# Optimization experiments

Measured on AMD Instinct MI355X. Metric: run time of the kernel, lower is better.

The kernel has to match this reference:

```python
import jax, jax.numpy as jnp
import numpy as np

B, T, N, H, DH = 32, 64, 100, 4, 32  # batch, seq, nodes, heads, dim/head


def setup_inputs() -> dict:
    key = jax.random.key(0)
    ks = jax.random.split(key, 20)
    # structured flat observation: [action_mask(132), adj(100*100), dt(1), obs(256), siem(128)]
    am = (jax.random.uniform(ks[0], (B, T, 132)) < 0.8).astype(jnp.float32)
    adj = (jax.random.uniform(ks[1], (B, T, N * N)) < 0.05).astype(jnp.float32)
    dt = jax.random.uniform(ks[2], (B, T, 1)) * 0.1 + 0.01
    obs = jax.random.normal(ks[3], (B, T, 256))
    siem = jax.random.normal(ks[4], (B, T, 128))
    inputs = jnp.concatenate([am, adj, dt, obs, siem], axis=-1)
    s = 0.05
    return dict(
        inputs=inputs,
        h0=jnp.zeros((B, 128), jnp.float32),
        fc_w=jax.random.normal(ks[5], (384, 256)) * s,
        fc_b=jnp.zeros((256,)),
        gat_w=jax.random.normal(ks[6], (256, H, DH)) * s,
        a_src=jax.random.normal(ks[7], (H, DH)) * s,
        a_dst=jax.random.normal(ks[8], (H, DH)) * s,
        ode_w1=jax.random.normal(ks[9], (128, 128)) * s,
        ode_b1=jnp.zeros((128,)),
        ode_w2=jax.random.normal(ks[10], (128, 128)) * s,
        ode_b2=jnp.zeros((128,)),
        gru_wi=jax.random.normal(ks[11], (128, 384)) * s,
        gru_wh=jax.random.normal(ks[12], (128, 384)) * s,
        gru_bi=jnp.zeros((384,)),
        gru_bh=jnp.zeros((384,)),
        act_w=jax.random.normal(ks[13], (128, 132)) * s,
        act_b=jnp.zeros((132,)),
        val_w=jax.random.normal(ks[14], (128, 1)) * s,
        val_b=jnp.zeros((1,)),
    )


def reference(inputs, h0, fc_w, fc_b, gat_w, a_src, a_dst, ode_w1, ode_b1,
              ode_w2, ode_b2, gru_wi, gru_wh, gru_bi, gru_bh, act_w, act_b,
              val_w, val_b):
    Bt, Tt = inputs.shape[0], inputs.shape[1]
    action_mask = inputs[..., :132]
    adj_raw = inputs[..., 132:10132].reshape(Bt * Tt, N, N)
    dtn = inputs[..., 10132:10133]                      # [B,T,1]
    x = jnp.concatenate([inputs[..., 10133:10389], inputs[..., 10389:10517]], -1)
    x = jax.nn.relu(x @ fc_w + fc_b).reshape(Bt * Tt, 256)
    # SubnetMaskGenerator.create_mask: binary adjacency + self loops
    adj = (adj_raw > 0) | jnp.eye(N, dtype=bool)[None]
    # place per-agent embedding at node 0, rest zero
    x_nodes = jnp.zeros((Bt * Tt, N, 256), x.dtype).at[:, 0, :].set(x)
    Wh = jnp.einsum('bnf,fhd->bhnd', x_nodes, gat_w)
    src = jnp.einsum('bhnd,hd->bhn', Wh, a_src)
    dst = jnp.einsum('bhnd,hd->bhn', Wh, a_dst)
    e = jax.nn.leaky_relu(src[:, :, :, None] + dst[:, :, None, :], 0.2)
    e = jnp.where(adj[:, None, :, :], e, -1e9)
    alpha = jax.nn.softmax(e, axis=-1)
    hgat = jax.nn.elu(jnp.einsum('bhij,bhjd->bhid', alpha, Wh))
    hgat = hgat.transpose(0, 2, 1, 3).reshape(Bt * Tt, N, H * DH)
    x_gat = hgat.mean(axis=1).reshape(Bt, Tt, 128)

    def f(h):  # ODE dynamics net
        return jnp.tanh(jnp.tanh(h @ ode_w1 + ode_b1) @ ode_w2 + ode_b2)

    def step(h, inp):
        xt, dt = inp                                    # [B,128], [B,1]
        k1 = f(h)
        k2 = f(h + 0.5 * dt * k1)
        k3 = f(h + 0.5 * dt * k2)
        k4 = f(h + dt * k3)
        h_ode = h + dt / 6.0 * (k1 + 2 * k2 + 2 * k3 + k4)
        gi = xt @ gru_wi + gru_bi
        gh = h_ode @ gru_wh + gru_bh
        ir, iz, inn = jnp.split(gi, 3, -1)
        hr, hz, hn = jnp.split(gh, 3, -1)
        r = jax.nn.sigmoid(ir + hr)
        z = jax.nn.sigmoid(iz + hz)
        n = jnp.tanh(inn + r * hn)
        h_new = (1.0 - z) * n + z * h_ode
        return h_new, h_new

    h_T, hs = jax.lax.scan(step, h0, (x_gat.transpose(1, 0, 2), dtn.transpose(1, 0, 2)))
    x_rnn = hs.transpose(1, 0, 2)                       # [B,T,128]
    logits = x_rnn @ act_w + act_b
    value = (x_rnn @ val_w + val_b).reshape(-1)
    masked_logits = jnp.where(action_mask == 0.0, jnp.float32(-1e10), logits)
    return masked_logits, h_T, value
```

## Files before the change

### kernel.cpp

```cpp
#include <hip/hip_runtime.h>

#define NIN 10517
typedef unsigned short ushort_t;
using f32x4  = __attribute__((ext_vector_type(4))) float;
using bf16x8 = __attribute__((ext_vector_type(8))) short;

__device__ __forceinline__ float lrelu02(float x){ return x > 0.f ? x : 0.2f*x; }
__device__ __forceinline__ float fast_tanh(float x){ float e=__expf(2.f*x); return 1.f - 2.f/(e+1.f); }
__device__ __forceinline__ float fast_sig(float x){ return 1.f/(1.f+__expf(-x)); }

__device__ __forceinline__ ushort_t f2bf(float x){
  unsigned u = __float_as_uint(x);
  unsigned r = u + 0x7FFF + ((u >> 16) & 1);
  return (ushort_t)(r >> 16);
}

#define LBAR() do { asm volatile("s_waitcnt lgkmcnt(0)" ::: "memory"); \
                    __builtin_amdgcn_s_barrier(); } while (0)

__global__ __launch_bounds__(256) void k_fc_gat(const float* __restrict__ inputs,
    const float* __restrict__ fc_w, const float* __restrict__ fc_b,
    const float* __restrict__ gat_w, const float* __restrict__ a_src, const float* __restrict__ a_dst,
    const float* __restrict__ ode_w1, const float* __restrict__ ode_w2, const float* __restrict__ gru_wh,
    float* __restrict__ wh0_ws, float* __restrict__ sd_ws,
    ushort_t* __restrict__ w1B, ushort_t* __restrict__ w2B, ushort_t* __restrict__ ghB)
{
  __shared__ float xin[16][384];
  __shared__ float xfc[16][256];
  __shared__ float wh[16][128];
  const int tid = threadIdx.x;
  const int bt0 = blockIdx.x * 16;

  {
    int gidx = blockIdx.x * 256 + tid;
    for (int idx = gidx; idx < 384*128; idx += 128*256) {
      int m = idx >> 7, k = idx & 127;
      ghB[idx] = f2bf(gru_wh[k*384 + m]);
    }
    if (gidx < 128*128) {
      int jj = gidx >> 7, k = gidx & 127;
      w1B[gidx] = f2bf(ode_w1[k*128 + jj]);
      w2B[gidx] = f2bf(ode_w2[k*128 + jj]);
    }
  }

  for (int idx = tid; idx < 16*384; idx += 256) {
    int r = idx / 384, f = idx - r*384;
    xin[r][f] = inputs[(size_t)(bt0+r)*NIN + 10133 + f];
  }
  __syncthreads();
  {
    float acc[16];
    float bj = fc_b[tid];
    #pragma unroll
    for (int r=0;r<16;r++) acc[r] = bj;
    for (int f=0; f<384; f++) {
      float wf = fc_w[f*256 + tid];
      #pragma unroll
      for (int r=0;r<16;r++) acc[r] = fmaf(xin[r][f], wf, acc[r]);
    }
    #pragma unroll
    for (int r=0;r<16;r++) xfc[r][tid] = fmaxf(acc[r], 0.f);
  }
  __syncthreads();
  {
    const int j2 = tid & 127, r0 = (tid >> 7) * 8;
    float acc[8];
    #pragma unroll
    for (int r=0;r<8;r++) acc[r] = 0.f;
    for (int f=0; f<256; f++) {
      float wf = gat_w[f*128 + j2];
      #pragma unroll
      for (int r=0;r<8;r++) acc[r] = fmaf(xfc[r0+r][f], wf, acc[r]);
    }
    #pragma unroll
    for (int r=0;r<8;r++) {
      wh[r0+r][j2] = acc[r];
      wh0_ws[(size_t)(bt0+r0+r)*128 + j2] = acc[r];
    }
  }
  __syncthreads();
  if (tid < 128) {
    const int r = tid >> 3, h = (tid >> 1) & 3, w = tid & 1;
    const float* av = w ? a_dst : a_src;
    float acc = 0.f;
    #pragma unroll
    for (int d=0; d<32; d++) acc = fmaf(wh[r][h*32+d], av[h*32+d], acc);
    sd_ws[(size_t)(bt0+r)*8 + w*4 + h] = acc;
  }
}

__global__ __launch_bounds__(256) void k_alpha_gi(const float* __restrict__ inputs,
    const float* __restrict__ wh0_ws, const float* __restrict__ sd_ws,
    const float* __restrict__ gru_wi, const float* __restrict__ gru_bi,
    float* __restrict__ gi_ws)
{
  __shared__ int cnt[100];
  __shared__ int a0f[100];
  __shared__ float alpha[4][100];
  __shared__ float wh0[128];
  __shared__ float sdl[8];
  __shared__ float xg[128];
  const int tid = threadIdx.x;
  const size_t bt = blockIdx.x;
  if (tid < 128) wh0[tid] = wh0_ws[bt*128 + tid];
  if (tid < 8) sdl[tid] = sd_ws[bt*8 + tid];
  const float* adj = inputs + bt*NIN + 132;
  const int wv = tid >> 6, lane = tid & 63;
  for (int i = wv; i < 100; i += 4) {
    float v0 = adj[i*100 + lane];
    int pred0 = (lane != 0) && ((v0 > 0.f) || (lane == i));
    unsigned long long b0 = __ballot(pred0);
    int pred1 = 0;
    if (lane < 36) {
      float v1 = adj[i*100 + 64 + lane];
      pred1 = (v1 > 0.f) || ((64 + lane) == i);
    }
    unsigned long long b1 = __ballot(pred1);
    if (lane == 0) {
      cnt[i] = __popcll(b0) + __popcll(b1);
      a0f[i] = (v0 > 0.f) ? 1 : 0;
    }
  }
  __syncthreads();
  for (int idx = tid; idx < 400; idx += 256) {
    int h = idx / 100, i = idx - h*100;
    float s = sdl[h], d = sdl[4+h];
    float a;
    if (i == 0) {
      float ea = __expf(lrelu02(s + d));
      float eb = __expf(lrelu02(s));
      a = ea / (ea + (float)cnt[0] * eb);
    } else if (a0f[i]) {
      float ed = __expf(lrelu02(d));
      a = ed / (ed + (float)cnt[i]);
    } else {
      a = 0.f;
    }
    alpha[h][i] = a;
  }
  __syncthreads();
  if (tid < 128) {
    const int h = tid >> 5;
    const float w = wh0[tid];
    float sum = 0.f;
    for (int i=0;i<100;i++) {
      float t = alpha[h][i] * w;
      sum += (t > 0.f) ? t : (__expf(t) - 1.f);
    }
    xg[tid] = sum * 0.01f;
  }
  __syncthreads();
  for (int jj = tid; jj < 384; jj += 256) {
    float acc = gru_bi[jj];
    for (int f=0; f<128; f++) acc = fmaf(xg[f], gru_wi[f*384 + jj], acc);
    gi_ws[bt*384 + jj] = acc;
  }
}

__global__ __launch_bounds__(512) void k_rnn(const float* __restrict__ inputs,
    const float* __restrict__ h0,
    const ushort_t* __restrict__ w1B, const float* __restrict__ ode_b1,
    const ushort_t* __restrict__ w2B, const float* __restrict__ ode_b2,
    const ushort_t* __restrict__ ghB, const float* __restrict__ gru_bh,
    const float* __restrict__ gi_ws, float* __restrict__ hs_ws, float* __restrict__ hT_out)
{
  __shared__ __align__(16) ushort_t bufA[128];
  __shared__ __align__(16) ushort_t bufB[128];
  __shared__ __align__(16) ushort_t bufC[128];
  __shared__ float dtbuf[64];
  const int tid = threadIdx.x;
  const int b = blockIdx.x;
  const int w = tid >> 6, lane = tid & 63;
  const int li = lane & 15, g = lane >> 4;
  const int col = w*16 + li;

  bf16x8 W1f[4], W2f[4], GAf[4], GBf[4], GCf[4];
  #pragma unroll
  for (int kt=0;kt<4;kt++){
    W1f[kt] = *reinterpret_cast<const bf16x8*>(w1B + col*128       + kt*32 + g*8);
    W2f[kt] = *reinterpret_cast<const bf16x8*>(w2B + col*128       + kt*32 + g*8);
    GAf[kt] = *reinterpret_cast<const bf16x8*>(ghB + (size_t)col*128         + kt*32 + g*8);
    GBf[kt] = *reinterpret_cast<const bf16x8*>(ghB + (size_t)(col+128)*128   + kt*32 + g*8);
    GCf[kt] = *reinterpret_cast<const bf16x8*>(ghB + (size_t)(col+256)*128   + kt*32 + g*8);
  }
  const float b1 = ode_b1[col], b2 = ode_b2[col];
  const float bh0 = gru_bh[col], bh1 = gru_bh[col+128], bh2 = gru_bh[col+256];
  float h = h0[b*128 + col];
  if (tid < 64) dtbuf[tid] = inputs[((size_t)b*64 + tid)*NIN + 10132];
  if (lane < 16) bufC[col] = f2bf(h);
  const float* gib = gi_ws + (size_t)b*64*384 + col;
  __syncthreads();

  auto MV = [&](const ushort_t* __restrict__ hb, const bf16x8 (&Wf)[4], float bias)->float {
    f32x4 acc = {0.f, 0.f, 0.f, 0.f};
    #pragma unroll
    for (int kt=0;kt<4;kt++){
      bf16x8 af = *reinterpret_cast<const bf16x8*>(hb + kt*32 + g*8);
      acc = __builtin_amdgcn_mfma_f32_16x16x32_bf16(af, Wf[kt], acc, 0, 0, 0);
    }
    return fast_tanh(acc[0] + bias);
  };

  for (int t=0; t<64; t++) {
    const float dt = dtbuf[t];
    const float gir = gib[(size_t)t*384];
    const float giz = gib[(size_t)t*384 + 128];
    const float gin = gib[(size_t)t*384 + 256];

    float u, k1, k2, k3, k4;
    u  = MV(bufC, W1f, b1); if (lane<16) bufA[col] = f2bf(u);                      LBAR();
    k1 = MV(bufA, W2f, b2); if (lane<16) bufB[col] = f2bf(fmaf(0.5f*dt, k1, h));   LBAR();
    u  = MV(bufB, W1f, b1); if (lane<16) bufA[col] = f2bf(u);                      LBAR();
    k2 = MV(bufA, W2f, b2); if (lane<16) bufB[col] = f2bf(fmaf(0.5f*dt, k2, h));   LBAR();
    u  = MV(bufB, W1f, b1); if (lane<16) bufA[col] = f2bf(u);                      LBAR();
    k3 = MV(bufA, W2f, b2); if (lane<16) bufB[col] = f2bf(fmaf(dt, k3, h));        LBAR();
    u  = MV(bufB, W1f, b1); if (lane<16) bufA[col] = f2bf(u);                      LBAR();
    k4 = MV(bufA, W2f, b2);
    const float h_ode = fmaf(dt*(1.f/6.f), (k1 + 2.f*k2) + (2.f*k3 + k4), h);
    if (lane<16) bufB[col] = f2bf(h_ode);                                          LBAR();

    {
      f32x4 a0 = {0.f,0.f,0.f,0.f}, a1 = {0.f,0.f,0.f,0.f}, a2 = {0.f,0.f,0.f,0.f};
      #pragma unroll
      for (int kt=0;kt<4;kt++){
        bf16x8 af = *reinterpret_cast<const bf16x8*>(bufB + kt*32 + g*8);
        a0 = __builtin_amdgcn_mfma_f32_16x16x32_bf16(af, GAf[kt], a0, 0, 0, 0);
        a1 = __builtin_amdgcn_mfma_f32_16x16x32_bf16(af, GBf[kt], a1, 0, 0, 0);
        a2 = __builtin_amdgcn_mfma_f32_16x16x32_bf16(af, GCf[kt], a2, 0, 0, 0);
      }
      const float r = fast_sig(gir + a0[0] + bh0);
      const float z = fast_sig(giz + a1[0] + bh1);
      const float n = fast_tanh(gin + r*(a2[0] + bh2));
      h = (1.f - z)*n + z*h_ode;
    }
    if (lane < 16) {
      bufC[col] = f2bf(h);
      hs_ws[((size_t)b*64 + t)*128 + col] = h;
    }
    LBAR();
  }
  if (lane < 16) hT_out[b*128 + col] = h;
}

__global__ __launch_bounds__(256) void k_head(const float* __restrict__ hs_ws,
    const float* __restrict__ act_w, const float* __restrict__ act_b,
    const float* __restrict__ val_w, const float* __restrict__ val_b,
    const float* __restrict__ inputs, float* __restrict__ out_logits, float* __restrict__ out_val)
{
  __shared__ float xr[16][128];
  const int tid = threadIdx.x;
  const int bt0 = blockIdx.x * 16;
  for (int idx = tid; idx < 16*128; idx += 256) {
    int r = idx >> 7, f = idx & 127;
    xr[r][f] = hs_ws[(size_t)(bt0+r)*128 + f];
  }
  __syncthreads();
  if (tid < 132) {
    float acc[16];
    float bj = act_b[tid];
    #pragma unroll
    for (int r=0;r<16;r++) acc[r] = bj;
    for (int f=0; f<128; f++) {
      float wf = act_w[f*132 + tid];
      #pragma unroll
      for (int r=0;r<16;r++) acc[r] = fmaf(xr[r][f], wf, acc[r]);
    }
    #pragma unroll
    for (int r=0;r<16;r++) {
      float mval = inputs[(size_t)(bt0+r)*NIN + tid];
      out_logits[(size_t)(bt0+r)*132 + tid] = (mval == 0.f) ? -1e10f : acc[r];
    }
  } else if (tid >= 136 && tid < 152) {
    int r = tid - 136;
    float acc = val_b[0];
    for (int f=0; f<128; f++) acc = fmaf(xr[r][f], val_w[f], acc);
    out_val[bt0 + r] = acc;
  }
}

extern "C" void kernel_launch(void* const* d_in, const int* in_sizes, int n_in,
                              void* d_out, int out_size, void* d_ws, size_t ws_size,
                              hipStream_t stream) {
  (void)in_sizes; (void)n_in; (void)out_size; (void)ws_size;
  const float* inputs = (const float*)d_in[0];
  const float* h0     = (const float*)d_in[1];
  const float* fc_w   = (const float*)d_in[2];
  const float* fc_b   = (const float*)d_in[3];
  const float* gat_w  = (const float*)d_in[4];
  const float* a_src  = (const float*)d_in[5];
  const float* a_dst  = (const float*)d_in[6];
  const float* ode_w1 = (const float*)d_in[7];
  const float* ode_b1 = (const float*)d_in[8];
  const float* ode_w2 = (const float*)d_in[9];
  const float* ode_b2 = (const float*)d_in[10];
  const float* gru_wi = (const float*)d_in[11];
  const float* gru_wh = (const float*)d_in[12];
  const float* gru_bi = (const float*)d_in[13];
  const float* gru_bh = (const float*)d_in[14];
  const float* act_w  = (const float*)d_in[15];
  const float* act_b  = (const float*)d_in[16];
  const float* val_w  = (const float*)d_in[17];
  const float* val_b  = (const float*)d_in[18];

  float* ws   = (float*)d_ws;
  float* wh0  = ws;
  float* sd   = ws + 262144;
  float* gi   = ws + 278528;
  float* hs   = ws + 1064960;
  ushort_t* w1B = (ushort_t*)(ws + 1327104);
  ushort_t* w2B = (ushort_t*)(ws + 1335296);
  ushort_t* ghB = (ushort_t*)(ws + 1343488);

  float* out        = (float*)d_out;
  float* out_logits = out;
  float* out_hT     = out + 270336;
  float* out_val    = out + 274432;

  k_fc_gat  <<<dim3(128),  dim3(256), 0, stream>>>(inputs, fc_w, fc_b, gat_w, a_src, a_dst,
                                                   ode_w1, ode_w2, gru_wh,
                                                   wh0, sd, w1B, w2B, ghB);
  k_alpha_gi<<<dim3(2048), dim3(256), 0, stream>>>(inputs, wh0, sd, gru_wi, gru_bi, gi);
  k_rnn     <<<dim3(32),   dim3(512), 0, stream>>>(inputs, h0, w1B, ode_b1, w2B, ode_b2,
                                                   ghB, gru_bh, gi, hs, out_hT);
  k_head    <<<dim3(128),  dim3(256), 0, stream>>>(hs, act_w, act_b, val_w, val_b, inputs,
                                                   out_logits, out_val);
}
```

Before: 242.0 us.

## Fuse output head into RNN kernel and restructure RNN to two columns per wave

Moves the action/value head into the recurrent kernel, keeping the hidden states in LDS as bf16 and computing logits with MFMA, which removes one launch and the global hs round trip. The RNN kernel now uses 4 waves that each own two 16-column tiles, with independent MFMA accumulators summed at the end to shorten dependency chains. The first kernel uses smaller 8-row tiles over 256 blocks, and the alpha reduction is split across all 256 threads. Logits and value are now computed from bf16 hidden states, which lowers precision, and more registers per thread may limit the RNN kernel.

```diff
diff --git a/kernel.cpp b/kernel.cpp
--- a/kernel.cpp
+++ b/kernel.cpp
@@ -14,6 +14,7 @@
   unsigned r = u + 0x7FFF + ((u >> 16) & 1);
   return (ushort_t)(r >> 16);
 }
+__device__ __forceinline__ float bf2f(ushort_t v){ return __uint_as_float(((unsigned)v) << 16); }
 
 #define LBAR() do { asm volatile("s_waitcnt lgkmcnt(0)" ::: "memory"); \
                     __builtin_amdgcn_s_barrier(); } while (0)
@@ -22,65 +23,70 @@
     const float* __restrict__ fc_w, const float* __restrict__ fc_b,
     const float* __restrict__ gat_w, const float* __restrict__ a_src, const float* __restrict__ a_dst,
     const float* __restrict__ ode_w1, const float* __restrict__ ode_w2, const float* __restrict__ gru_wh,
+    const float* __restrict__ act_w,
     float* __restrict__ wh0_ws, float* __restrict__ sd_ws,
-    ushort_t* __restrict__ w1B, ushort_t* __restrict__ w2B, ushort_t* __restrict__ ghB)
+    ushort_t* __restrict__ w1B, ushort_t* __restrict__ w2B, ushort_t* __restrict__ ghB,
+    ushort_t* __restrict__ actB)
 {
-  __shared__ float xin[16][384];
-  __shared__ float xfc[16][256];
-  __shared__ float wh[16][128];
+  __shared__ float xin[8][384];
+  __shared__ float xfc[8][256];
+  __shared__ float wh[8][128];
   const int tid = threadIdx.x;
-  const int bt0 = blockIdx.x * 16;
-
-  {
-    int gidx = blockIdx.x * 256 + tid;
-    for (int idx = gidx; idx < 384*128; idx += 128*256) {
-      int m = idx >> 7, k = idx & 127;
-      ghB[idx] = f2bf(gru_wh[k*384 + m]);
-    }
-    if (gidx < 128*128) {
-      int jj = gidx >> 7, k = gidx & 127;
-      w1B[gidx] = f2bf(ode_w1[k*128 + jj]);
-      w2B[gidx] = f2bf(ode_w2[k*128 + jj]);
-    }
-  }
-
-  for (int idx = tid; idx < 16*384; idx += 256) {
+  const int bt0 = blockIdx.x * 8;
+
+  for (int p = blockIdx.x * 256 + tid; p < 100352; p += 256*256) {
+    if (p < 49152) {
+      int m = p >> 7, k = p & 127;
+      ghB[p] = f2bf(gru_wh[k*384 + m]);
+    } else if (p < 65536) {
+      int q = p - 49152, jj = q >> 7, k = q & 127;
+      w1B[q] = f2bf(ode_w1[k*128 + jj]);
+    } else if (p < 81920) {
+      int q = p - 65536, jj = q >> 7, k = q & 127;
+      w2B[q] = f2bf(ode_w2[k*128 + jj]);
+    } else {
+      int q = p - 81920, col = q >> 7, k = q & 127;
+      actB[q] = (col < 132) ? f2bf(act_w[k*132 + col]) : (ushort_t)0;
+    }
+  }
+
+  for (int idx = tid; idx < 8*384; idx += 256) {
     int r = idx / 384, f = idx - r*384;
     xin[r][f] = inputs[(size_t)(bt0+r)*NIN + 10133 + f];
   }
   __syncthreads();
   {
-    float acc[16];
+    float acc[8];
     float bj = fc_b[tid];
     #pragma unroll
-    for (int r=0;r<16;r++) acc[r] = bj;
+    for (int r=0;r<8;r++) acc[r] = bj;
     for (int f=0; f<384; f++) {
       float wf = fc_w[f*256 + tid];
       #pragma unroll
-      for (int r=0;r<16;r++) acc[r] = fmaf(xin[r][f], wf, acc[r]);
-    }
-    #pragma unroll
-    for (int r=0;r<16;r++) xfc[r][tid] = fmaxf(acc[r], 0.f);
+      for (int r=0;r<8;r++) acc[r] = fmaf(xin[r][f], wf, acc[r]);
+    }
+    #pragma unroll
+    for (int r=0;r<8;r++) xfc[r][tid] = fmaxf(acc[r], 0.f);
   }
   __syncthreads();
   {
-    const int j2 = tid & 127, r0 = (tid >> 7) * 8;
-    float acc[8];
-    #pragma unroll
-    for (int r=0;r<8;r++) acc[r] = 0.f;
+    const int j2 = tid & 127, r0 = (tid >> 7) * 4;
+    float acc[4];
+    #pragma unroll
+    for (int r=0;r<4;r++) acc[r] = 0.f;
     for (int f=0; f<256; f++) {
       float wf = gat_w[f*128 + j2];
       #pragma unroll
-      for (int r=0;r<8;r++) acc[r] = fmaf(xfc[r0+r][f], wf, acc[r]);
-    }
-    #pragma unroll
-    for (int r=0;r<8;r++) {
+      for (int r=0;r<4;r++) acc[r] = fmaf(xfc[r0+r][f], wf, acc[r]);
+    }
+    #pragma unroll
+    for (int r=0;r<4;r++) {
       wh[r0+r][j2] = acc[r];
       wh0_ws[(size_t)(bt0+r0+r)*128 + j2] = acc[r];
     }
   }
   __syncthreads();
-  if (tid < 128) {
+  if (tid < 64) {
     const int r = tid >> 3, h = (tid >> 1) & 3, w = tid & 1;
     const float* av = w ? a_dst : a_src;
     float acc = 0.f;
@@ -101,6 +107,7 @@
   __shared__ float wh0[128];
   __shared__ float sdl[8];
   __shared__ float xg[128];
+  __shared__ float psum[256];
   const int tid = threadIdx.x;
   const size_t bt = blockIdx.x;
   if (tid < 128) wh0[tid] = wh0_ws[bt*128 + tid];
@@ -140,16 +147,20 @@
     alpha[h][i] = a;
   }
   __syncthreads();
-  if (tid < 128) {
-    const int h = tid >> 5;
-    const float w = wh0[tid];
+  {
+    const int pr = tid & 127, hf = tid >> 7;
+    const float w = wh0[pr];
+    const int hh = pr >> 5;
     float sum = 0.f;
-    for (int i=0;i<100;i++) {
-      float t = alpha[h][i] * w;
+    const int i0 = hf * 50;
+    for (int i = i0; i < i0 + 50; i++) {
+      float t = alpha[hh][i] * w;
       sum += (t > 0.f) ? t : (__expf(t) - 1.f);
     }
-    xg[tid] = sum * 0.01f;
-  }
+    psum[tid] = sum;
+  }
+  __syncthreads();
+  if (tid < 128) xg[tid] = (psum[tid] + psum[tid+128]) * 0.01f;
   __syncthreads();
   for (int jj = tid; jj < 384; jj += 256) {
     float acc = gru_bi[jj];
@@ -158,124 +169,145 @@
   }
 }
 
-__global__ __launch_bounds__(512) void k_rnn(const float* __restrict__ inputs,
+__global__ __launch_bounds__(256) void k_rnn(const float* __restrict__ inputs,
     const float* __restrict__ h0,
     const ushort_t* __restrict__ w1B, const float* __restrict__ ode_b1,
     const ushort_t* __restrict__ w2B, const float* __restrict__ ode_b2,
     const ushort_t* __restrict__ ghB, const float* __restrict__ gru_bh,
-    const float* __restrict__ gi_ws, float* __restrict__ hs_ws, float* __restrict__ hT_out)
+    const ushort_t* __restrict__ actB, const float* __restrict__ act_b,
+    const float* __restrict__ val_w, const float* __restrict__ val_b,
+    const float* __restrict__ gi_ws,
+    float* __restrict__ out_logits, float* __restrict__ out_hT, float* __restrict__ out_val)
 {
   __shared__ __align__(16) ushort_t bufA[128];
   __shared__ __align__(16) ushort_t bufB[128];
   __shared__ __align__(16) ushort_t bufC[128];
   __shared__ float dtbuf[64];
+  __shared__ __align__(16) ushort_t hsbuf[64*136];
   const int tid = threadIdx.x;
   const int b = blockIdx.x;
   const int w = tid >> 6, lane = tid & 63;
   const int li = lane & 15, g = lane >> 4;
-  const int col = w*16 + li;
-
-  bf16x8 W1f[4], W2f[4], GAf[4], GBf[4], GCf[4];
+  const int colA = (2*w)*16 + li, colB = colA + 16;
+
+  bf16x8 W1A[4], W1Bf[4], W2A[4], W2Bf[4];
+  bf16x8 GAA[4], GAB[4], GBA[4], GBB[4], GCA[4], GCB[4];
   #pragma unroll
   for (int kt=0;kt<4;kt++){
-    W1f[kt] = *reinterpret_cast<const bf16x8*>(w1B + col*128       + kt*32 + g*8);
-    W2f[kt] = *reinterpret_cast<const bf16x8*>(w2B + col*128       + kt*32 + g*8);
-    GAf[kt] = *reinterpret_cast<const bf16x8*>(ghB + (size_t)col*128         + kt*32 + g*8);
-    GBf[kt] = *reinterpret_cast<const bf16x8*>(ghB + (size_t)(col+128)*128   + kt*32 + g*8);
-    GCf[kt] = *reinterpret_cast<const bf16x8*>(ghB + (size_t)(col+256)*128   + kt*32 + g*8);
-  }
-  const float b1 = ode_b1[col], b2 = ode_b2[col];
-  const float bh0 = gru_bh[col], bh1 = gru_bh[col+128], bh2 = gru_bh[col+256];
-  float h = h0[b*128 + col];
+    const int o = kt*32 + g*8;
+    W1A[kt]  = *reinterpret_cast<const bf16x8*>(w1B + colA*128 + o);
+    W1Bf[kt] = *reinterpret_cast<const bf16x8*>(w1B + colB*128 + o);
+    W2A[kt]  = *reinterpret_cast<const bf16x8*>(w2B + colA*128 + o);
+    W2Bf[kt] = *reinterpret_cast<const bf16x8*>(w2B + colB*128 + o);
+    GAA[kt]  = *reinterpret_cast<const bf16x8*>(ghB + (size_t)colA*128 + o);
+    GAB[kt]  = *reinterpret_cast<const bf16x8*>(ghB + (size_t)colB*128 + o);
+    GBA[kt]  = *reinterpret_cast<const bf16x8*>(ghB + (size_t)(colA+128)*128 + o);
+    GBB[kt]  = *reinterpret_cast<const bf16x8*>(ghB + (size_t)(colB+128)*128 + o);
+    GCA[kt]  = *reinterpret_cast<const bf16x8*>(ghB + (size_t)(colA+256)*128 + o);
+    GCB[kt]  = *reinterpret_cast<const bf16x8*>(ghB + (size_t)(colB+256)*128 + o);
+  }
+  const float b1A = ode_b1[colA], b1B = ode_b1[colB];
+  const float b2A = ode_b2[colA], b2B = ode_b2[colB];
+  const float bh0A = gru_bh[colA],     bh0B = gru_bh[colB];
+  const float bh1A = gru_bh[colA+128], bh1B = gru_bh[colB+128];
+  const float bh2A = gru_bh[colA+256], bh2B = gru_bh[colB+256];
+  float hA = h0[b*128 + colA], hB = h0[b*128 + colB];
   if (tid < 64) dtbuf[tid] = inputs[((size_t)b*64 + tid)*NIN + 10132];
-  if (lane < 16) bufC[col] = f2bf(h);
-  const float* gib = gi_ws + (size_t)b*64*384 + col;
-  __syncthreads();
-
-  auto MV = [&](const ushort_t* __restrict__ hb, const bf16x8 (&Wf)[4], float bias)->float {
-    f32x4 acc = {0.f, 0.f, 0.f, 0.f};
-    #pragma unroll
-    for (int kt=0;kt<4;kt++){
-      bf16x8 af = *reinterpret_cast<const bf16x8*>(hb + kt*32 + g*8);
-      acc = __builtin_amdgcn_mfma_f32_16x16x32_bf16(af, Wf[kt], acc, 0, 0, 0);
-    }
-    return fast_tanh(acc[0] + bias);
+  if (g == 0) { bufC[colA] = f2bf(hA); bufC[colB] = f2bf(hB); }
+  const float* gibA = gi_ws + (size_t)b*64*384 + colA;
+  const float* gibB = gi_ws + (size_t)b*64*384 + colB;
+  __syncthreads();
+
+  bf16x8 af[4];
+  auto ldaf = [&](const ushort_t* __restrict__ hb){
+    #pragma unroll
+    for (int kt=0;kt<4;kt++) af[kt] = *reinterpret_cast<const bf16x8*>(hb + kt*32 + g*8);
+  };
+  auto mvac = [&](const bf16x8 (&Wf)[4])->float{
+    const f32x4 z0 = {0.f,0.f,0.f,0.f};
+    f32x4 c0 = __builtin_amdgcn_mfma_f32_16x16x32_bf16(af[0], Wf[0], z0, 0,0,0);
+    f32x4 c1 = __builtin_amdgcn_mfma_f32_16x16x32_bf16(af[1], Wf[1], z0, 0,0,0);
+    f32x4 c2 = __builtin_amdgcn_mfma_f32_16x16x32_bf16(af[2], Wf[2], z0, 0,0,0);
+    f32x4 c3 = __builtin_amdgcn_mfma_f32_16x16x32_bf16(af[3], Wf[3], z0, 0,0,0);
+    return (c0[0]+c1[0]) + (c2[0]+c3[0]);
   };
 
   for (int t=0; t<64; t++) {
     const float dt = dtbuf[t];
-    const float gir = gib[(size_t)t*384];
-    const float giz = gib[(size_t)t*384 + 128];
-    const float gin = gib[(size_t)t*384 + 256];
-
-    float u, k1, k2, k3, k4;
-    u  = MV(bufC, W1f, b1); if (lane<16) bufA[col] = f2bf(u);                      LBAR();
-    k1 = MV(bufA, W2f, b2); if (lane<16) bufB[col] = f2bf(fmaf(0.5f*dt, k1, h));   LBAR();
-    u  = MV(bufB, W1f, b1); if (lane<16) bufA[col] = f2bf(u);                      LBAR();
-    k2 = MV(bufA, W2f, b2); if (lane<16) bufB[col] = f2bf(fmaf(0.5f*dt, k2, h));   LBAR();
-    u  = MV(bufB, W1f, b1); if (lane<16) bufA[col] = f2bf(u);                      LBAR();
-    k3 = MV(bufA, W2f, b2); if (lane<16) bufB[col] = f2bf(fmaf(dt, k3, h));        LBAR();
-    u  = MV(bufB, W1f, b1); if (lane<16) bufA[col] = f2bf(u);                      LBAR();
-    k4 = MV(bufA, W2f, b2);
-    const float h_ode = fmaf(dt*(1.f/6.f), (k1 + 2.f*k2) + (2.f*k3 + k4), h);
-    if (lane<16) bufB[col] = f2bf(h_ode);                                          LBAR();
-
+    const float girA = gibA[(size_t)t*384], gizA = gibA[(size_t)t*384+128], ginA = gibA[(size_t)t*384+256];
+    const float girB = gibB[(size_t)t*384], gizB = gibB[(size_t)t*384+128], ginB = gibB[(size_t)t*384+256];
+    float uA, uB, k1A, k1B, k2A, k2B, k3A, k3B, k4A, k4B;
+
+    ldaf(bufC); uA = fast_tanh(mvac(W1A)+b1A); uB = fast_tanh(mvac(W1Bf)+b1B);
+    if (!g){ bufA[colA]=f2bf(uA); bufA[colB]=f2bf(uB); }                                 LBAR();
+    ldaf(bufA); k1A = fast_tanh(mvac(W2A)+b2A); k1B = fast_tanh(mvac(W2Bf)+b2B);
+    if (!g){ bufB[colA]=f2bf(fmaf(0.5f*dt,k1A,hA)); bufB[colB]=f2bf(fmaf(0.5f*dt,k1B,hB)); } LBAR();
+    ldaf(bufB); uA = fast_tanh(mvac(W1A)+b1A); uB = fast_tanh(mvac(W1Bf)+b1B);
+    if (!g){ bufA[colA]=f2bf(uA); bufA[colB]=f2bf(uB); }                                 LBAR();
+    ldaf(bufA); k2A = fast_tanh(mvac(W2A)+b2A); k2B = fast_tanh(mvac(W2Bf)+b2B);
+    if (!g){ bufB[colA]=f2bf(fmaf(0.5f*dt,k2A,hA)); bufB[colB]=f2bf(fmaf(0.5f*dt,k2B,hB)); } LBAR();
+    ldaf(bufB); uA = fast_tanh(mvac(W1A)+b1A); uB = fast_tanh(mvac(W1Bf)+b1B);
+    if (!g){ bufA[colA]=f2bf(uA); bufA[colB]=f2bf(uB); }                                 LBAR();
+    ldaf(bufA); k3A = fast_tanh(mvac(W2A)+b2A); k3B = fast_tanh(mvac(W2Bf)+b2B);
+    if (!g){ bufB[colA]=f2bf(fmaf(dt,k3A,hA)); bufB[colB]=f2bf(fmaf(dt,k3B,hB)); }       LBAR();
+    ldaf(bufB); uA = fast_tanh(mvac(W1A)+b1A); uB = fast_tanh(mvac(W1Bf)+b1B);
+    if (!g){ bufA[colA]=f2bf(uA); bufA[colB]=f2bf(uB); }                                 LBAR();
+    ldaf(bufA); k4A = fast_tanh(mvac(W2A)+b2A); k4B = fast_tanh(mvac(W2Bf)+b2B);
+    const float hoA = fmaf(dt*(1.f/6.f), (k1A + 2.f*k2A) + (2.f*k3A + k4A), hA);
+    const float hoB = fmaf(dt*(1.f/6.f), (k1B + 2.f*k2B) + (2.f*k3B + k4B), hB);
+    if (!g){ bufB[colA]=f2bf(hoA); bufB[colB]=f2bf(hoB); }                               LBAR();
+
+    ldaf(bufB);
     {
-      f32x4 a0 = {0.f,0.f,0.f,0.f}, a1 = {0.f,0.f,0.f,0.f}, a2 = {0.f,0.f,0.f,0.f};
+      const float rA = fast_sig(girA + mvac(GAA) + bh0A);
+      const float rB = fast_sig(girB + mvac(GAB) + bh0B);
+      const float zA = fast_sig(gizA + mvac(GBA) + bh1A);
+      const float zB = fast_sig(gizB + mvac(GBB) + bh1B);
+      const float nA = fast_tanh(ginA + rA*(mvac(GCA) + bh2A));
+      const float nB = fast_tanh(ginB + rB*(mvac(GCB) + bh2B));
+      hA = (1.f - zA)*nA + zA*hoA;
+      hB = (1.f - zB)*nB + zB*hoB;
+    }
+    if (!g){
+      bufC[colA] = f2bf(hA);           bufC[colB] = f2bf(hB);
+      hsbuf[t*136 + colA] = f2bf(hA);  hsbuf[t*136 + colB] = f2bf(hB);
+    }
+    LBAR();
+  }
+
+  if (!g){ out_hT[b*128 + colA] = hA; out_hT[b*128 + colB] = hB; }
+
+  {
+    const int r0 = w*16;
+    bf16x8 haf[4];
+    #pragma unroll
+    for (int kt=0;kt<4;kt++)
+      haf[kt] = *reinterpret_cast<const bf16x8*>(hsbuf + (r0+li)*136 + kt*32 + g*8);
+    #pragma unroll
+    for (int ct=0; ct<9; ct++){
+      f32x4 acc = {0.f,0.f,0.f,0.f};
       #pragma unroll
       for (int kt=0;kt<4;kt++){
-        bf16x8 af = *reinterpret_cast<const bf16x8*>(bufB + kt*32 + g*8);
-        a0 = __builtin_amdgcn_mfma_f32_16x16x32_bf16(af, GAf[kt], a0, 0, 0, 0);
-        a1 = __builtin_amdgcn_mfma_f32_16x16x32_bf16(af, GBf[kt], a1, 0, 0, 0);
-        a2 = __builtin_amdgcn_mfma_f32_16x16x32_bf16(af, GCf[kt], a2, 0, 0, 0);
+        bf16x8 bfr = *reinterpret_cast<const bf16x8*>(actB + (size_t)(ct*16+li)*128 + kt*32 + g*8);
+        acc = __builtin_amdgcn_mfma_f32_16x16x32_bf16(haf[kt], bfr, acc, 0,0,0);
       }
-      const float r = fast_sig(gir + a0[0] + bh0);
-      const float z = fast_sig(giz + a1[0] + bh1);
-      const float n = fast_tanh(gin + r*(a2[0] + bh2));
-      h = (1.f - z)*n + z*h_ode;
-    }
-    if (lane < 16) {
-      bufC[col] = f2bf(h);
-      hs_ws[((size_t)b*64 + t)*128 + col] = h;
-    }
-    LBAR();
-  }
-  if (lane < 16) hT_out[b*128 + col] = h;
-}
-
-__global__ __launch_bounds__(256) void k_head(const float* __restrict__ hs_ws,
-    const float* __restrict__ act_w, const float* __restrict__ act_b,
-    const float* __restrict__ val_w, const float* __restrict__ val_b,
-    const float* __restrict__ inputs, float* __restrict__ out_logits, float* __restrict__ out_val)
-{
-  __shared__ float xr[16][128];
-  const int tid = threadIdx.x;
-  const int bt0 = blockIdx.x * 16;
-  for (int idx = tid; idx < 16*128; idx += 256) {
-    int r = idx >> 7, f = idx & 127;
-    xr[r][f] = hs_ws[(size_t)(bt0+r)*128 + f];
-  }
-  __syncthreads();
-  if (tid < 132) {
-    float acc[16];
-    float bj = act_b[tid];
-    #pragma unroll
-    for (int r=0;r<16;r++) acc[r] = bj;
-    for (int f=0; f<128; f++) {
-      float wf = act_w[f*132 + tid];
-      #pragma unroll
-      for (int r=0;r<16;r++) acc[r] = fmaf(xr[r][f], wf, acc[r]);
-    }
-    #pragma unroll
-    for (int r=0;r<16;r++) {
-      float mval = inputs[(size_t)(bt0+r)*NIN + tid];
-      out_logits[(size_t)(bt0+r)*132 + tid] = (mval == 0.f) ? -1e10f : acc[r];
-    }
-  } else if (tid >= 136 && tid < 152) {
-    int r = tid - 136;
+      const int col = ct*16 + li;
+      if (col < 132){
+        const float ab = act_b[col];
+        #pragma unroll
+        for (int reg=0; reg<4; reg++){
+          const int r = r0 + g*4 + reg;
+          const size_t bt = (size_t)b*64 + r;
+          const float mval = inputs[bt*NIN + col];
+          out_logits[bt*132 + col] = (mval == 0.f) ? -1e10f : (acc[reg] + ab);
+        }
+      }
+    }
+  }
+  if (tid < 64){
     float acc = val_b[0];
-    for (int f=0; f<128; f++) acc = fmaf(xr[r][f], val_w[f], acc);
-    out_val[bt0 + r] = acc;
+    for (int k=0;k<128;k++) acc = fmaf(bf2f(hsbuf[tid*136 + k]), val_w[k], acc);
+    out_val[b*64 + tid] = acc;
   }
 }
 
@@ -307,22 +339,21 @@
   float* wh0  = ws;
   float* sd   = ws + 262144;
   float* gi   = ws + 278528;
-  float* hs   = ws + 1064960;
-  ushort_t* w1B = (ushort_t*)(ws + 1327104);
-  ushort_t* w2B = (ushort_t*)(ws + 1335296);
-  ushort_t* ghB = (ushort_t*)(ws + 1343488);
+  ushort_t* w1B  = (ushort_t*)(ws + 1064960);
+  ushort_t* w2B  = (ushort_t*)(ws + 1073152);
+  ushort_t* ghB  = (ushort_t*)(ws + 1081344);
+  ushort_t* actB = (ushort_t*)(ws + 1105920);
 
   float* out        = (float*)d_out;
   float* out_logits = out;
   float* out_hT     = out + 270336;
   float* out_val    = out + 274432;
 
-  k_fc_gat  <<<dim3(128),  dim3(256), 0, stream>>>(inputs, fc_w, fc_b, gat_w, a_src, a_dst,
-                                                   ode_w1, ode_w2, gru_wh,
-                                                   wh0, sd, w1B, w2B, ghB);
+  k_fc_gat  <<<dim3(256),  dim3(256), 0, stream>>>(inputs, fc_w, fc_b, gat_w, a_src, a_dst,
+                                                   ode_w1, ode_w2, gru_wh, act_w,
+                                                   wh0, sd, w1B, w2B, ghB, actB);
   k_alpha_gi<<<dim3(2048), dim3(256), 0, stream>>>(inputs, wh0, sd, gru_wi, gru_bi, gi);
-  k_rnn     <<<dim3(32),   dim3(512), 0, stream>>>(inputs, h0, w1B, ode_b1, w2B, ode_b2,
-                                                   ghB, gru_bh, gi, hs, out_hT);
-  k_head    <<<dim3(128),  dim3(256), 0, stream>>>(hs, act_w, act_b, val_w, val_b, inputs,
-                                                   out_logits, out_val);
-}
+  k_rnn     <<<dim3(32),   dim3(256), 0, stream>>>(inputs, h0, w1B, ode_b1, w2B, ode_b2,
+                                                   ghB, gru_bh, actB, act_b, val_w, val_b,
+                                                   gi, out_logits, out_hT, out_val);
+}
```

Result: slower. 259.7 us (+7.3%).
